# Performance work log

Hardware: AMD Instinct MI355X
Metric: run time of the kernel (lower is better)

Reference implementation:

```python
import jax, jax.numpy as jnp
import numpy as np

WS = 32          # window_size
STRIDE = 16
OUTPUT = 224
GRADE_N = 6

def _dct_mat(size):
    i = np.arange(size)[:, None]
    j = np.arange(size)[None, :]
    scale = np.where(i == 0, np.sqrt(1.0 / size), np.sqrt(2.0 / size))
    return (scale * np.cos((j + 0.5) * np.pi * i / size)).astype(np.float32)

def _gen_filter(start, end, size):
    i = np.arange(size)[:, None]
    j = np.arange(size)[None, :]
    s = i + j
    return np.where((s > end) | (s < start), 0.0, 1.0).astype(np.float32)

# constant (non-learnable) buffers, derived from init hyperparams
_D = jnp.asarray(_dct_mat(WS))                       # [32,32]
_LEVEL_FILT = jnp.asarray(_gen_filter(0, WS * 2, WS))  # level_fliter=[0] -> band (0, 64)
_grade_filts = np.stack([_gen_filter(WS * 2.0 / GRADE_N * i, WS * 2.0 / GRADE_N * (i + 1), WS)
                         for i in range(GRADE_N)])    # [G,32,32]
_ft_num = _grade_filts.sum(axis=(1, 2))               # per-filter normalizer
_weights = (2.0 ** np.arange(GRADE_N)).astype(np.float32)  # w=1, *=2 each pass
_GRADE_FILT_SCALED = jnp.asarray(_grade_filts * (_weights / _ft_num)[:, None, None])  # [G,32,32]

def _unfold(x):
    # x: [B,C,H,W] -> patches [B,L,C,ws,ws], L row-major over (oh, ow), matching torch Unfold
    B, C, H, W = x.shape
    nH = (H - WS) // STRIDE + 1
    nW = (W - WS) // STRIDE + 1
    r = jnp.arange(nH) * STRIDE
    c = jnp.arange(nW) * STRIDE
    rows = r[:, None, None, None] + jnp.arange(WS)[None, None, :, None]  # [nH,1,ws,1]
    cols = c[None, :, None, None] + jnp.arange(WS)[None, None, None, :]  # [1,nW,1,ws]
    p = x[:, :, rows, cols]                       # [B,C,nH,nW,ws,ws]
    p = jnp.transpose(p, (0, 2, 3, 1, 4, 5))      # [B,nH,nW,C,ws,ws]
    return p.reshape(B, nH * nW, C, WS, WS)

def setup_inputs() -> dict:
    key = jax.random.key(0)
    x = jax.random.normal(key, (16, 3, 512, 512), dtype=jnp.float32)
    return {"x": x}

def reference(x):
    B, C, H, W = x.shape
    patches = _unfold(x)                          # [B,L,C,32,32]
    x_dct = _D @ patches @ _D.T                   # batched 32x32 DCT

    # level branch (level_N=1): filter is all-pass band (0,64) but applied faithfully
    level_y = _D.T @ (x_dct * _LEVEL_FILT) @ _D   # [B,L,C,32,32]

    # grading: sum_g w_g/ft_g * sum_{c,i,j} filt_g * log(|dct|+1)
    lx = jnp.log(jnp.abs(x_dct) + 1.0)
    grade = jnp.einsum('blcij,gij->bl', lx, _GRADE_FILT_SCALED)  # [B,L]

    idx = jnp.argsort(grade, axis=-1)             # ascending
    b = jnp.arange(B)
    minmin_i  = idx[:, 0]
    minmin_i1 = idx[:, 1]    # B > 1 branch
    maxmax_i  = idx[:, -1]
    maxmax_i1 = idx[:, -2]   # B > 1 branch

    # gather single patch per image; fold0 with one block == reshape to [B,C,32,32]
    x_minmin  = level_y[b, minmin_i]
    x_maxmax  = level_y[b, maxmax_i]
    x_minmin1 = level_y[b, minmin_i1]
    x_maxmax1 = level_y[b, maxmax_i1]
    return (x_minmin, x_maxmax, x_minmin1, x_maxmax1)
```

## Files before the change

### kernel.cpp

```cpp
#include <hip/hip_runtime.h>
#include <cstdint>

typedef _Float16 f16x8 __attribute__((ext_vector_type(8)));
typedef float    f32x4 __attribute__((ext_vector_type(4)));

constexpr double kPI  = 3.14159265358979323846264338327950288;
constexpr double kLN2 = 0.69314718055994530941723212145818;
constexpr double cos_poly(double x) {
    double x2 = x * x, term = 1.0, sum = 1.0;
    for (int n = 1; n <= 13; ++n) { term *= -x2 / double((2 * n - 1) * (2 * n)); sum += term; }
    return sum;
}
constexpr double cos_idx(int a) {
    a &= 127;
    if (a <= 32)  return  cos_poly(a * kPI / 64.0);
    if (a <= 64)  return -cos_poly((64 - a) * kPI / 64.0);
    if (a <= 96)  return -cos_poly((a - 64) * kPI / 64.0);
    return cos_poly((128 - a) * kPI / 64.0);
}
constexpr double csqrt(double v) {
    double x = 1.0;
    for (int i = 0; i < 60; ++i) x = 0.5 * (x + v / x);
    return x;
}
struct DTab { float d[1024]; };
constexpr DTab make_D() {
    DTab t{};
    const double s0 = csqrt(1.0 / 32.0);
    for (int i = 0; i < 32; ++i) {
        double sc = (i == 0) ? s0 : 0.25;
        for (int j = 0; j < 32; ++j)
            t.d[i * 32 + j] = (float)(sc * cos_idx(((2 * j + 1) * i) & 127));
    }
    return t;
}
struct FTab { float f[64]; };
constexpr FTab make_F() {
    FTab t{};
    const int lo[6] = {0, 11, 22, 32, 43, 54};
    const int hi[6] = {10, 21, 32, 42, 53, 62};
    const int n [6] = {66, 187, 306, 286, 165, 45};
    for (int s = 0; s < 64; ++s) {
        double acc = 0.0, w = 1.0;
        for (int g = 0; g < 6; ++g) { if (s >= lo[g] && s <= hi[g]) acc += w / double(n[g]); w *= 2.0; }
        t.f[s] = (float)(acc * kLN2);
    }
    return t;
}
__device__ constexpr DTab cD = make_D();
__device__ constexpr FTab cF = make_F();

#define NP  15376
#define NPC 46128
#define LPB 961
#define TP  36

__global__ __launch_bounds__(128) void k_init(_Float16* __restrict__ dfrag) {
    const int t = threadIdx.x;
    const int tile = t >> 6, lane = t & 63;
    const int m  = 16 * tile + (lane & 15);
    const int k0 = ((lane >> 4) & 3) * 8;
    #pragma unroll
    for (int j = 0; j < 8; ++j)
        dfrag[t * 8 + j] = (_Float16)cD.d[m * 32 + k0 + j];
}

__global__ __launch_bounds__(128, 4) void k_grade(const float* __restrict__ x,
                                                  const _Float16* __restrict__ dfrag,
                                                  float* __restrict__ partial) {
    __shared__ __align__(16) float sT[2][32 * TP];
    __shared__ float sF[64];
    const int tid  = threadIdx.x;
    const int wv   = tid >> 6, lane = tid & 63;
    const int quad = lane >> 4, n = lane & 15;
    if (tid < 64) sF[tid] = cF.f[tid];

    const int tc   = blockIdx.x * 2 + wv;
    const int task = tc / 3, c = tc - task * 3;
    const int b  = task / LPB, l = task - b * LPB;
    const int ph = l / 31, pw = l - ph * 31;

    const f16x8* DF = (const f16x8*)dfrag;
    const f16x8 d0 = DF[lane], d1 = DF[64 + lane];

    const float* pp = x + (size_t)(b * 3 + c) * 262144
                        + (size_t)(ph * 16 + quad * 8) * 512 + pw * 16 + n;
    f16x8 p0, p1;
    #pragma unroll
    for (int j = 0; j < 8; ++j) {
        p0[j] = (_Float16)pp[j * 512];
        p1[j] = (_Float16)pp[j * 512 + 16];
    }

    const f32x4 z4 = {0.f, 0.f, 0.f, 0.f};
    f32x4 t00 = __builtin_amdgcn_mfma_f32_16x16x32_f16(d0, p0, z4, 0, 0, 0);
    f32x4 t01 = __builtin_amdgcn_mfma_f32_16x16x32_f16(d0, p1, z4, 0, 0, 0);
    f32x4 t10 = __builtin_amdgcn_mfma_f32_16x16x32_f16(d1, p0, z4, 0, 0, 0);
    f32x4 t11 = __builtin_amdgcn_mfma_f32_16x16x32_f16(d1, p1, z4, 0, 0, 0);

    float* S = sT[wv];
    #pragma unroll
    for (int r = 0; r < 4; ++r) {
        S[(quad * 4 + r) * TP + n]           = t00[r];
        S[(quad * 4 + r) * TP + 16 + n]      = t01[r];
        S[(16 + quad * 4 + r) * TP + n]      = t10[r];
        S[(16 + quad * 4 + r) * TP + 16 + n] = t11[r];
    }
    __syncthreads();

    f16x8 a0, a1;
    {
        const float* rp = &S[n * TP + quad * 8];
        const float4 x0 = *(const float4*)(rp);
        const float4 x1 = *(const float4*)(rp + 4);
        const float4 x2 = *(const float4*)(rp + 16 * TP);
        const float4 x3 = *(const float4*)(rp + 16 * TP + 4);
        a0[0]=(_Float16)x0.x; a0[1]=(_Float16)x0.y; a0[2]=(_Float16)x0.z; a0[3]=(_Float16)x0.w;
        a0[4]=(_Float16)x1.x; a0[5]=(_Float16)x1.y; a0[6]=(_Float16)x1.z; a0[7]=(_Float16)x1.w;
        a1[0]=(_Float16)x2.x; a1[1]=(_Float16)x2.y; a1[2]=(_Float16)x2.z; a1[3]=(_Float16)x2.w;
        a1[4]=(_Float16)x3.x; a1[5]=(_Float16)x3.y; a1[6]=(_Float16)x3.z; a1[7]=(_Float16)x3.w;
    }

    f32x4 q00 = __builtin_amdgcn_mfma_f32_16x16x32_f16(a0, d0, z4, 0, 0, 0);
    f32x4 q01 = __builtin_amdgcn_mfma_f32_16x16x32_f16(a0, d1, z4, 0, 0, 0);
    f32x4 q10 = __builtin_amdgcn_mfma_f32_16x16x32_f16(a1, d0, z4, 0, 0, 0);
    f32x4 q11 = __builtin_amdgcn_mfma_f32_16x16x32_f16(a1, d1, z4, 0, 0, 0);

    const int sb = quad * 4 + n;
    float W[12];
    #pragma unroll
    for (int t2 = 0; t2 < 3; ++t2)
        #pragma unroll
        for (int r = 0; r < 4; ++r) W[t2 * 4 + r] = sF[sb + 16 * t2 + r];

    float gsum = 0.f;
    #pragma unroll
    for (int r = 0; r < 4; ++r) {
        gsum = fmaf(__log2f(fabsf(q00[r]) + 1.f), W[r],     gsum);
        gsum = fmaf(__log2f(fabsf(q01[r]) + 1.f), W[4 + r], gsum);
        gsum = fmaf(__log2f(fabsf(q10[r]) + 1.f), W[4 + r], gsum);
        gsum = fmaf(__log2f(fabsf(q11[r]) + 1.f), W[8 + r], gsum);
    }
    #pragma unroll
    for (int off = 32; off > 0; off >>= 1) gsum += __shfl_down(gsum, off, 64);
    if (lane == 0) partial[tc] = gsum;
}

__global__ __launch_bounds__(256) void k_selgather(const float* __restrict__ partial,
                                                   const float* __restrict__ x,
                                                   float* __restrict__ out) {
    __shared__ unsigned long long smx1[256], smx2[256], smn1[256], smn2[256];
    __shared__ int ssel[4];
    const int b = blockIdx.x, tid = threadIdx.x;
    unsigned long long mx1 = 0, mx2 = 0, mn1 = ~0ULL, mn2 = ~0ULL;
    for (int l = tid; l < LPB; l += 256) {
        const float* pp = partial + (size_t)(b * LPB + l) * 3;
        float gr = pp[0] + pp[1] + pp[2];
        unsigned int bits = __float_as_uint(gr);
        unsigned long long k = ((unsigned long long)bits << 32) | (unsigned int)l;
        if (k > mx1) { mx2 = mx1; mx1 = k; } else if (k > mx2) { mx2 = k; }
        if (k < mn1) { mn2 = mn1; mn1 = k; } else if (k < mn2) { mn2 = k; }
    }
    smx1[tid] = mx1; smx2[tid] = mx2; smn1[tid] = mn1; smn2[tid] = mn2;
    for (int off = 128; off > 0; off >>= 1) {
        __syncthreads();
        if (tid < off) {
            unsigned long long a1 = smx1[tid], a2 = smx2[tid], b1 = smx1[tid + off], b2 = smx2[tid + off];
            unsigned long long lo = a1 < b1 ? a1 : b1, hi = a1 < b1 ? b1 : a1;
            unsigned long long c2 = a2 > b2 ? a2 : b2;
            smx1[tid] = hi; smx2[tid] = lo > c2 ? lo : c2;
            a1 = smn1[tid]; a2 = smn2[tid]; b1 = smn1[tid + off]; b2 = smn2[tid + off];
            lo = a1 < b1 ? a1 : b1; hi = a1 < b1 ? b1 : a1;
            c2 = a2 < b2 ? a2 : b2;
            smn1[tid] = lo; smn2[tid] = hi < c2 ? hi : c2;
        }
    }
    __syncthreads();
    if (tid == 0) {
        ssel[0] = (int)(smn1[0] & 0xffffffffu);
        ssel[1] = (int)(smx1[0] & 0xffffffffu);
        ssel[2] = (int)(smn2[0] & 0xffffffffu);
        ssel[3] = (int)(smx2[0] & 0xffffffffu);
    }
    __syncthreads();

    #pragma unroll
    for (int it = 0; it < 12; ++it) {
        const int q  = it * 256 + tid;
        const int o  = q / 768;
        const int r2 = q - o * 768;
        const int c  = r2 >> 8;
        const int p  = r2 & 255;
        const int i  = p >> 3, j4 = p & 7;
        const int l  = ssel[o];
        const int r0 = (l / 31) * 16, c0 = (l - (l / 31) * 31) * 16;
        const float4 v = *(const float4*)(x + ((size_t)(b * 3 + c) * 512 + r0 + i) * 512 + c0 + 4 * j4);
        *(float4*)(out + (size_t)o * 49152 + b * 3072 + c * 1024 + i * 32 + 4 * j4) = v;
    }
}

extern "C" void kernel_launch(void* const* d_in, const int* in_sizes, int n_in,
                              void* d_out, int out_size, void* d_ws, size_t ws_size,
                              hipStream_t stream) {
    const float* x = (const float*)d_in[0];
    float* out     = (float*)d_out;
    float* partial = (float*)d_ws;
    _Float16* dfrag = (_Float16*)((char*)d_ws + 47104 * 4);
    k_init     <<<1,       128, 0, stream>>>(dfrag);
    k_grade    <<<NPC / 2, 128, 0, stream>>>(x, dfrag, partial);
    k_selgather<<<16,      256, 0, stream>>>(partial, x, out);
}
```

Measured before the change: 106.1 us.

## Vectorize patch loads, bake fp16 DCT fragments, split select and gather

The grading kernel now reads each patch as row-contiguous float4 loads instead of strided scalar loads. This feeds the transposed patch into the first MFMA, which is valid because the grade filter depends only on i+j and is therefore symmetric. The fp16 DCT fragment table is built at compile time, which removes the init kernel launch and its workspace round trip. The select-and-gather kernel is split into a 16-block selection kernel and a gather kernel with a 12x16 grid, spreading the output copy across more blocks at the cost of one extra launch.

```diff
diff --git a/kernel.cpp b/kernel.cpp
--- a/kernel.cpp
+++ b/kernel.cpp
@@ -23,15 +23,35 @@
     for (int i = 0; i < 60; ++i) x = 0.5 * (x + v / x);
     return x;
 }
-struct DTab { float d[1024]; };
-constexpr DTab make_D() {
-    DTab t{};
+constexpr unsigned short d2h(double dv) {
+    float f = (float)dv;
+    double v = (double)f;
+    unsigned short s = 0;
+    if (v < 0.0) { s = 0x8000; v = -v; }
+    if (v == 0.0) return s;
+    int e = 0;
+    while (v >= 2.0) { v *= 0.5; ++e; }
+    while (v < 1.0)  { v *= 2.0; --e; }
+    double m = (v - 1.0) * 1024.0;
+    int mi = (int)m;
+    double fr = m - (double)mi;
+    if (fr > 0.5 || (fr == 0.5 && (mi & 1))) ++mi;
+    int ef = e + 15;
+    if (mi == 1024) { mi = 0; ++ef; }
+    return (unsigned short)(s | (ef << 10) | mi);
+}
+struct __align__(16) HTab { unsigned short h[1024]; };
+constexpr HTab make_H() {
+    HTab t{};
     const double s0 = csqrt(1.0 / 32.0);
-    for (int i = 0; i < 32; ++i) {
-        double sc = (i == 0) ? s0 : 0.25;
-        for (int j = 0; j < 32; ++j)
-            t.d[i * 32 + j] = (float)(sc * cos_idx(((2 * j + 1) * i) & 127));
-    }
+    for (int tl = 0; tl < 2; ++tl)
+        for (int lane = 0; lane < 64; ++lane) {
+            const int m  = 16 * tl + (lane & 15);
+            const int k0 = (lane >> 4) * 8;
+            const double sc = (m == 0) ? s0 : 0.25;
+            for (int j = 0; j < 8; ++j)
+                t.h[(tl * 64 + lane) * 8 + j] = d2h(sc * cos_idx(((2 * (k0 + j) + 1) * m) & 127));
+        }
     return t;
 }
 struct FTab { float f[64]; };
@@ -47,7 +67,7 @@
     }
     return t;
 }
-__device__ constexpr DTab cD = make_D();
+__device__ constexpr HTab cH = make_H();
 __device__ constexpr FTab cF = make_F();
 
 #define NP  15376
@@ -55,18 +75,7 @@
 #define LPB 961
 #define TP  36
 
-__global__ __launch_bounds__(128) void k_init(_Float16* __restrict__ dfrag) {
-    const int t = threadIdx.x;
-    const int tile = t >> 6, lane = t & 63;
-    const int m  = 16 * tile + (lane & 15);
-    const int k0 = ((lane >> 4) & 3) * 8;
-    #pragma unroll
-    for (int j = 0; j < 8; ++j)
-        dfrag[t * 8 + j] = (_Float16)cD.d[m * 32 + k0 + j];
-}
-
 __global__ __launch_bounds__(128, 4) void k_grade(const float* __restrict__ x,
-                                                  const _Float16* __restrict__ dfrag,
                                                   float* __restrict__ partial) {
     __shared__ __align__(16) float sT[2][32 * TP];
     __shared__ float sF[64];
@@ -80,17 +89,20 @@
     const int b  = task / LPB, l = task - b * LPB;
     const int ph = l / 31, pw = l - ph * 31;
 
-    const f16x8* DF = (const f16x8*)dfrag;
+    const f16x8* DF = (const f16x8*)cH.h;
     const f16x8 d0 = DF[lane], d1 = DF[64 + lane];
 
     const float* pp = x + (size_t)(b * 3 + c) * 262144
-                        + (size_t)(ph * 16 + quad * 8) * 512 + pw * 16 + n;
+                        + (size_t)(ph * 16 + n) * 512 + pw * 16 + quad * 8;
+    const float4 v0 = *(const float4*)(pp);
+    const float4 v1 = *(const float4*)(pp + 4);
+    const float4 v2 = *(const float4*)(pp + 16 * 512);
+    const float4 v3 = *(const float4*)(pp + 16 * 512 + 4);
     f16x8 p0, p1;
-    #pragma unroll
-    for (int j = 0; j < 8; ++j) {
-        p0[j] = (_Float16)pp[j * 512];
-        p1[j] = (_Float16)pp[j * 512 + 16];
-    }
+    p0[0]=(_Float16)v0.x; p0[1]=(_Float16)v0.y; p0[2]=(_Float16)v0.z; p0[3]=(_Float16)v0.w;
+    p0[4]=(_Float16)v1.x; p0[5]=(_Float16)v1.y; p0[6]=(_Float16)v1.z; p0[7]=(_Float16)v1.w;
+    p1[0]=(_Float16)v2.x; p1[1]=(_Float16)v2.y; p1[2]=(_Float16)v2.z; p1[3]=(_Float16)v2.w;
+    p1[4]=(_Float16)v3.x; p1[5]=(_Float16)v3.y; p1[6]=(_Float16)v3.z; p1[7]=(_Float16)v3.w;
 
     const f32x4 z4 = {0.f, 0.f, 0.f, 0.f};
     f32x4 t00 = __builtin_amdgcn_mfma_f32_16x16x32_f16(d0, p0, z4, 0, 0, 0);
@@ -146,11 +158,9 @@
     if (lane == 0) partial[tc] = gsum;
 }
 
-__global__ __launch_bounds__(256) void k_selgather(const float* __restrict__ partial,
-                                                   const float* __restrict__ x,
-                                                   float* __restrict__ out) {
+__global__ __launch_bounds__(256) void k_select(const float* __restrict__ partial,
+                                                int* __restrict__ sel) {
     __shared__ unsigned long long smx1[256], smx2[256], smn1[256], smn2[256];
-    __shared__ int ssel[4];
     const int b = blockIdx.x, tid = threadIdx.x;
     unsigned long long mx1 = 0, mx2 = 0, mn1 = ~0ULL, mn2 = ~0ULL;
     for (int l = tid; l < LPB; l += 256) {
@@ -177,26 +187,28 @@
     }
     __syncthreads();
     if (tid == 0) {
-        ssel[0] = (int)(smn1[0] & 0xffffffffu);
-        ssel[1] = (int)(smx1[0] & 0xffffffffu);
-        ssel[2] = (int)(smn2[0] & 0xffffffffu);
-        ssel[3] = (int)(smx2[0] & 0xffffffffu);
-    }
-    __syncthreads();
-
-    #pragma unroll
-    for (int it = 0; it < 12; ++it) {
-        const int q  = it * 256 + tid;
-        const int o  = q / 768;
-        const int r2 = q - o * 768;
-        const int c  = r2 >> 8;
-        const int p  = r2 & 255;
-        const int i  = p >> 3, j4 = p & 7;
-        const int l  = ssel[o];
-        const int r0 = (l / 31) * 16, c0 = (l - (l / 31) * 31) * 16;
-        const float4 v = *(const float4*)(x + ((size_t)(b * 3 + c) * 512 + r0 + i) * 512 + c0 + 4 * j4);
-        *(float4*)(out + (size_t)o * 49152 + b * 3072 + c * 1024 + i * 32 + 4 * j4) = v;
-    }
+        sel[b * 4 + 0] = (int)(smn1[0] & 0xffffffffu);
+        sel[b * 4 + 1] = (int)(smx1[0] & 0xffffffffu);
+        sel[b * 4 + 2] = (int)(smn2[0] & 0xffffffffu);
+        sel[b * 4 + 3] = (int)(smx2[0] & 0xffffffffu);
+    }
+}
+
+__global__ __launch_bounds__(256) void k_gather(const int* __restrict__ sel,
+                                                const float* __restrict__ x,
+                                                float* __restrict__ out) {
+    const int b = blockIdx.y;
+    const int q = blockIdx.x * 256 + threadIdx.x;
+    const int o  = q / 768;
+    const int r2 = q - o * 768;
+    const int c  = r2 >> 8;
+    const int p  = r2 & 255;
+    const int i  = p >> 3, j4 = p & 7;
+    const int l  = sel[b * 4 + o];
+    const int lh = l / 31;
+    const int r0 = lh * 16, c0 = (l - lh * 31) * 16;
+    const float4 v = *(const float4*)(x + ((size_t)(b * 3 + c) * 512 + r0 + i) * 512 + c0 + 4 * j4);
+    *(float4*)(out + (size_t)o * 49152 + b * 3072 + c * 1024 + i * 32 + 4 * j4) = v;
 }
 
 extern "C" void kernel_launch(void* const* d_in, const int* in_sizes, int n_in,
@@ -205,8 +217,8 @@
     const float* x = (const float*)d_in[0];
     float* out     = (float*)d_out;
     float* partial = (float*)d_ws;
-    _Float16* dfrag = (_Float16*)((char*)d_ws + 47104 * 4);
-    k_init     <<<1,       128, 0, stream>>>(dfrag);
-    k_grade    <<<NPC / 2, 128, 0, stream>>>(x, dfrag, partial);
-    k_selgather<<<16,      256, 0, stream>>>(partial, x, out);
-}
+    int* sel       = (int*)((char*)d_ws + NPC * 4);
+    k_grade <<<NPC / 2,     128, 0, stream>>>(x, partial);
+    k_select<<<16,          256, 0, stream>>>(partial, sel);
+    k_gather<<<dim3(12,16), 256, 0, stream>>>(sel, x, out);
+}
```

New measurement: 104.5 us. No clear change (-1.6%).
